# Performance work log

Hardware: AMD Instinct MI355X
Metric: run time of the kernel (lower is better)

## Reference

```python
import jax, jax.numpy as jnp
import numpy as np

U, B, I, D = 50000, 20000, 40000, 64
E_UI, E_UB, E_UBX, E_AGG = 1000000, 600000, 800000, 300000
EPS = 1e-8


def _bip_graph(rng, nA, nB, nE):
    """Symmetric Laplacian-normalized bipartite graph as directed COO edge list."""
    r = rng.integers(0, nA, nE)
    c = rng.integers(0, nB, nE)
    deg_r = np.bincount(r, minlength=nA).astype(np.float32)
    deg_c = np.bincount(c, minlength=nB).astype(np.float32)
    v = (1.0 / (np.sqrt(deg_r[r]) + EPS)) * (1.0 / (np.sqrt(deg_c[c]) + EPS))
    rows = np.concatenate([r, c + nA])
    cols = np.concatenate([c + nA, r])
    vals = np.concatenate([v, v]).astype(np.float32)
    return np.stack([rows, cols]).astype(np.int32), vals


def setup_inputs() -> dict:
    rng = np.random.default_rng(0)
    ui_idx, ui_val = _bip_graph(rng, U, I, E_UI)
    ub_idx, ub_val = _bip_graph(rng, U, B, E_UB)
    ubx_idx, ubx_val = _bip_graph(rng, U, B, E_UBX)  # ingredient-augmented u-b graph
    # bundle aggregation graph: row-normalized B x I (bi graph)
    br = rng.integers(0, B, E_AGG)
    bc = rng.integers(0, I, E_AGG)
    bdeg = np.bincount(br, minlength=B).astype(np.float32)
    agg_val = (1.0 / np.maximum(bdeg[br], 1.0)).astype(np.float32)
    agg_idx = np.stack([br, bc]).astype(np.int32)
    key = jax.random.key(0)
    ku, kb, ki = jax.random.split(key, 3)
    s = np.sqrt(2.0 / (U + D)).astype(np.float32)  # xavier-normal-ish scale
    return {
        "users_feature": jax.random.normal(ku, (U, D), jnp.float32) * 0.02,
        "bundles_feature": jax.random.normal(kb, (B, D), jnp.float32) * 0.02,
        "items_feature": jax.random.normal(ki, (I, D), jnp.float32) * 0.02,
        "ui_idx": jnp.asarray(ui_idx), "ui_val": jnp.asarray(ui_val),
        "ub_idx": jnp.asarray(ub_idx), "ub_val": jnp.asarray(ub_val),
        "ubx_idx": jnp.asarray(ubx_idx), "ubx_val": jnp.asarray(ubx_val),
        "agg_idx": jnp.asarray(agg_idx), "agg_val": jnp.asarray(agg_val),
        "num_layers": 2,
    }


def _spmm(idx, val, x, n_out):
    # y[r] += val[e] * x[c] for each edge e=(r,c)
    return jax.ops.segment_sum(val[:, None] * x[idx[1]], idx[0], num_segments=n_out)


def _l2norm(x):
    n = jnp.sqrt(jnp.sum(x * x, axis=1, keepdims=True))
    return x / jnp.maximum(n, 1e-12)


def _one_propagate(idx, val, A_feat, B_feat, num_layers):
    feats = jnp.concatenate([A_feat, B_feat], axis=0)
    n = feats.shape[0]
    acc = feats  # layer 0 raw
    f = feats
    for i in range(num_layers):
        f = _spmm(idx, val, f, n) / (i + 2)
        acc = acc + _l2norm(f)
    return acc[: A_feat.shape[0]], acc[A_feat.shape[0]:]


def reference(users_feature, bundles_feature, items_feature, ui_idx, ui_val,
              ub_idx, ub_val, ubx_idx, ubx_val, agg_idx, agg_val, num_layers):
    # item-level propagation over user-item graph
    IL_u, IL_i = _one_propagate(ui_idx, ui_val, users_feature, items_feature, num_layers)
    IL_b = _spmm(agg_idx, agg_val, IL_i, bundles_feature.shape[0])  # bundle agg from items
    # bundle-level propagation over user-bundle graph
    BL_u, BL_b = _one_propagate(ub_idx, ub_val, users_feature, bundles_feature, num_layers)
    # ingredient-augmented user-bundle propagation
    XL_u, XL_b = _one_propagate(ubx_idx, ubx_val, users_feature, bundles_feature, num_layers)
    # pack all representations: [3*U + 3*B, D]
    return jnp.concatenate([IL_u, BL_u, XL_u, IL_b, BL_b, XL_b], axis=0)
```

## Files before the change

### kernel.cpp

```cpp
#include <hip/hip_runtime.h>

#define D 64
constexpr int U_ = 50000, B_ = 20000, I_ = 40000;
constexpr int RPB  = 128;
constexpr int MAXB = 708;
constexpr int PTILE = 8192;

constexpr int NBU = 390;
constexpr int CAPU_UI = 3584, CAPB_UI = 4352;
constexpr int CAPA    = 2560;
constexpr int CAPU_UB = 2432, CAPB_UB = 4864;
constexpr int CAPU_UX = 2944, CAPB_UX = 6272;
constexpr int EXT_UI = NBU * CAPU_UI + 314 * CAPB_UI;
constexpr int EXT_AG = 157 * CAPA;
constexpr int EXT_UB = NBU * CAPU_UB + 157 * CAPB_UB;
constexpr int EXT_UX = NBU * CAPU_UX + 157 * CAPB_UX;
constexpr long long EXT_SUM = (long long)EXT_UI + EXT_AG + EXT_UB + EXT_UX;

__device__ __forceinline__ int g_nbU(int seg) { return seg == 1 ? 0 : NBU; }
__device__ __forceinline__ int g_capU(int seg) {
    switch (seg) { case 0: return CAPU_UI; case 1: return CAPA;
                   case 2: return CAPU_UB; default: return CAPU_UX; }
}
__device__ __forceinline__ int g_capB(int seg) {
    switch (seg) { case 0: return CAPB_UI; case 1: return CAPA;
                   case 2: return CAPB_UB; default: return CAPB_UX; }
}
__device__ __forceinline__ int bbase(int seg, int b) {
    int nbU = g_nbU(seg);
    return (b <= nbU) ? b * g_capU(seg)
                      : nbU * g_capU(seg) + (b - nbU) * g_capB(seg);
}

__device__ __forceinline__ unsigned short f2bf(float f) {
    unsigned int u = __float_as_uint(f);
    return (unsigned short)((u + 0x7FFFu + ((u >> 16) & 1u)) >> 16);
}

struct GD {
    const int* rows; const int* cols;
    int* ep; int* cnt; int* bktcur;
    int* ecol; int* rowstart; int* rowend; float* scale;
    const float* rawA; const float* rawB_adj;
    ushort* fb;
    int nnz, G, nbuck, seg, n, mode, do_pad, do_stage;
};
struct GB4 { GD g[4]; int ng; int Gpre[5]; int nbpre[5]; };

__global__ void __launch_bounds__(256) k_cntB(GB4 P) {
    __shared__ int lcnt[MAXB];
    int blk = blockIdx.x, t = threadIdx.x;
    int gi = 0;
    while (gi + 1 < P.ng && blk >= P.Gpre[gi + 1]) gi++;
    const GD& d = P.g[gi];
    int rel = blk - P.Gpre[gi];
    const int* __restrict__ rows = d.rows;
    for (int i = t; i < d.nbuck; i += 256) lcnt[i] = 0;
    __syncthreads();
    int e0 = rel * PTILE, e1 = min(e0 + PTILE, d.nnz);
    int e = e0 + t;
    for (; e + 1792 < e1; e += 2048) {
        int r[8];
        #pragma unroll
        for (int k = 0; k < 8; k++) r[k] = rows[e + k * 256];
        #pragma unroll
        for (int k = 0; k < 8; k++) atomicAdd(&lcnt[r[k] >> 7], 1);
    }
    for (; e < e1; e += 256) atomicAdd(&lcnt[rows[e] >> 7], 1);
    __syncthreads();
    for (int b = t; b < d.nbuck; b += 256) d.cnt[(size_t)b * d.G + rel] = lcnt[b];
}

__global__ void __launch_bounds__(256) k_scanB(GB4 P) {
    __shared__ int sv[256];
    int bk = blockIdx.x, t = threadIdx.x;
    int gi = 0;
    while (gi + 1 < P.ng && bk >= P.nbpre[gi + 1]) gi++;
    const GD& d = P.g[gi];
    int rel = bk - P.nbpre[gi];
    int x = (t < d.G) ? d.cnt[(size_t)rel * d.G + t] : 0;
    sv[t] = x;
    __syncthreads();
    for (int off = 1; off < 256; off <<= 1) {
        int y = (t >= off) ? sv[t - off] : 0;
        __syncthreads();
        sv[t] += y;
        __syncthreads();
    }
    int bb = bbase(d.seg, rel);
    if (t < d.G) d.cnt[(size_t)rel * d.G + t] = bb + sv[t] - x;
    if (t == 255) d.bktcur[rel] = bb + sv[255];
}

__global__ void __launch_bounds__(256) k_scatB(GB4 P) {
    __shared__ int lbase[MAXB], lcnt[MAXB], llim[MAXB];
    int blk = blockIdx.x, t = threadIdx.x;
    int gi = 0;
    while (gi + 1 < P.ng && blk >= P.Gpre[gi + 1]) gi++;
    const GD& d = P.g[gi];
    int rel = blk - P.Gpre[gi];
    const int* __restrict__ rows = d.rows;
    const int* __restrict__ cols = d.cols;
    int* __restrict__ ep = d.ep;
    for (int b = t; b < d.nbuck; b += 256) {
        lbase[b] = d.cnt[(size_t)b * d.G + rel];
        llim[b]  = bbase(d.seg, b + 1);
        lcnt[b]  = 0;
    }
    __syncthreads();
    int e0 = rel * PTILE, e1 = min(e0 + PTILE, d.nnz);
    int e = e0 + t;
    for (; e + 1792 < e1; e += 2048) {
        int r[8], c[8];
        #pragma unroll
        for (int k = 0; k < 8; k++) { r[k] = rows[e + k * 256]; c[k] = cols[e + k * 256]; }
        #pragma unroll
        for (int k = 0; k < 8; k++) {
            int b = r[k] >> 7;
            int pos = lbase[b] + atomicAdd(&lcnt[b], 1);
            if (pos < llim[b])
                ep[pos] = ((r[k] & (RPB - 1)) << 17) | c[k];
        }
    }
    for (; e < e1; e += 256) {
        int r = rows[e], c = cols[e];
        int b = r >> 7;
        int pos = lbase[b] + atomicAdd(&lcnt[b], 1);
        if (pos < llim[b])
            ep[pos] = ((r & (RPB - 1)) << 17) | c;
    }
}

__global__ void __launch_bounds__(256) k_sortB(GB4 P) {
    __shared__ int lc[4 * 129];
    __shared__ float sscale[RPB];
    __shared__ int wtot;
    int bk = blockIdx.x, t = threadIdx.x;
    int gi = 0;
    while (gi + 1 < P.ng && bk >= P.nbpre[gi + 1]) gi++;
    const GD& d = P.g[gi];
    int b = bk - P.nbpre[gi];
    const int* __restrict__ ep = d.ep;
    int* __restrict__ ecol = d.ecol;
    int s = bbase(d.seg, b);
    int e = min(d.bktcur[b], bbase(d.seg, b + 1));
    int ne = e - s;
    for (int i = t; i < 4 * 129; i += 256) lc[i] = 0;
    __syncthreads();
    int rep = (t & 3) * 129;
    int i = t;
    for (; i + 768 < ne; i += 1024) {
        int p0 = ep[s+i], p1 = ep[s+i+256], p2 = ep[s+i+512], p3 = ep[s+i+768];
        atomicAdd(&lc[rep + (p0 >> 17)], 1); atomicAdd(&lc[rep + (p1 >> 17)], 1);
        atomicAdd(&lc[rep + (p2 >> 17)], 1); atomicAdd(&lc[rep + (p3 >> 17)], 1);
    }
    for (; i < ne; i += 256) { int p = ep[s + i]; atomicAdd(&lc[rep + (p >> 17)], 1); }
    __syncthreads();
    int c_t = 0, pc_t = 0, v = 0;
    if (t < RPB) {
        c_t = lc[t] + lc[129 + t] + lc[258 + t] + lc[387 + t];
        pc_t = d.do_pad ? ((c_t + 7) & ~7) : c_t;
        v = pc_t;
        for (int off = 1; off < 64; off <<= 1) {
            int y = __shfl_up(v, off, 64);
            if ((t & 63) >= off) v += y;
        }
    }
    if (t == 63) wtot = v;
    __syncthreads();
    if (t >= 64 && t < RPB) v += wtot;
    if (t < RPB) {
        int row = b * RPB + t;
        if (row < d.n) {
            int st = s + (v - pc_t);
            d.rowstart[row] = st;
            d.rowend[row]   = st + pc_t;
            float sc = (d.mode == 0) ? 1.0f / (sqrtf((float)c_t) + 1e-8f)
                                     : 1.0f / (float)max(c_t, 1);
            d.scale[row] = sc;
            sscale[t] = sc;
            for (int k = c_t; k < pc_t; k++) ecol[st + k] = d.n;
            lc[t] = st;
        } else lc[t] = 0;
    }
    __syncthreads();
    i = t;
    for (; i + 768 < ne; i += 1024) {
        int p0 = ep[s+i], p1 = ep[s+i+256], p2 = ep[s+i+512], p3 = ep[s+i+768];
        int q0 = atomicAdd(&lc[p0 >> 17], 1); ecol[q0] = p0 & 0x1FFFF;
        int q1 = atomicAdd(&lc[p1 >> 17], 1); ecol[q1] = p1 & 0x1FFFF;
        int q2 = atomicAdd(&lc[p2 >> 17], 1); ecol[q2] = p2 & 0x1FFFF;
        int q3 = atomicAdd(&lc[p3 >> 17], 1); ecol[q3] = p3 & 0x1FFFF;
    }
    for (; i < ne; i += 256) {
        int p = ep[s + i];
        int q = atomicAdd(&lc[p >> 17], 1);
        ecol[q] = p & 0x1FFFF;
    }
    if (d.do_stage) {
        int r0 = b * RPB;
        for (int idx = t; idx < RPB * 16; idx += 256) {
            int rl = idx >> 4, q = idx & 15;
            int row = r0 + rl;
            if (row > d.n) continue;
            ushort4 o;
            if (row == d.n) {
                o = make_ushort4(0, 0, 0, 0);
            } else {
                float sc = sscale[rl];
                float4 vv = (row < U_) ? ((const float4*)d.rawA)[(size_t)row * 16 + q]
                                       : ((const float4*)d.rawB_adj)[(size_t)row * 16 + q];
                o.x = f2bf(vv.x * sc); o.y = f2bf(vv.y * sc);
                o.z = f2bf(vv.z * sc); o.w = f2bf(vv.w * sc);
            }
            ((ushort4*)d.fb)[(size_t)row * 16 + q] = o;
        }
    }
}

struct LD {
    const int* rowstart; const int* rowend; const float* scale;
    const int* ecol; const ushort* x; ushort* fout;
    const float* rawA; const float* rawB_adj;
    float* accA; float* accB;
    float inv; int n, write_f, init;
};
struct LB3 { LD l[3]; int nl; int qpre[4]; };

__global__ void __launch_bounds__(256) k_layerB(LB3 P) {
    int blk = blockIdx.x;
    int gi = 0;
    while (gi + 1 < P.nl && blk >= P.qpre[gi + 1]) gi++;
    const LD& d = P.l[gi];
    int rel = blk - P.qpre[gi];
    if (d.write_f && rel == 0 && threadIdx.x < 16)
        ((ushort4*)(d.fout + ((size_t)d.n << 6)))[threadIdx.x] = make_ushort4(0, 0, 0, 0);
    const int* __restrict__ rowstart = d.rowstart;
    const int* __restrict__ rowend   = d.rowend;
    const int* __restrict__ ecol     = d.ecol;
    const float* __restrict__ scale  = d.scale;
    const uint4* __restrict__ xb = (const uint4*)d.x;
    const int lane = threadIdx.x & 63;
    const int qtr  = lane >> 4;
    const int ql   = lane & 15;
    const int g = ql >> 3, q = ql & 7;
    int rowA = (rel << 4) + ((threadIdx.x >> 6) << 2);
    if (rowA >= d.n) return;
    int row = rowA + qtr;
    int s = 0, e = 0;
    if (row < d.n) { s = rowstart[row]; e = rowend[row]; }
    float a0=0.f,a1=0.f,a2=0.f,a3=0.f,a4=0.f,a5=0.f,a6=0.f,a7=0.f;
#define LDQ(m, vv) { int c_ = __shfl(cj, (qtr << 4) + ((m) << 1) + g, 64); \
                     vv = xb[((size_t)(unsigned)c_ << 3) + (unsigned)q]; }
#define ACCQ(vv) { \
    a0 += __uint_as_float(vv.x << 16); a1 += __uint_as_float(vv.x & 0xFFFF0000u); \
    a2 += __uint_as_float(vv.y << 16); a3 += __uint_as_float(vv.y & 0xFFFF0000u); \
    a4 += __uint_as_float(vv.z << 16); a5 += __uint_as_float(vv.z & 0xFFFF0000u); \
    a6 += __uint_as_float(vv.w << 16); a7 += __uint_as_float(vv.w & 0xFFFF0000u); }
    for (int base = s; base < e; base += 16) {
        int jn = e - base;
        int cj = ecol[base + ql];
        uint4 v0, v1, v2, v3, v4, v5, v6, v7;
        if (jn >= 16) {
            LDQ(0, v0); LDQ(1, v1); LDQ(2, v2); LDQ(3, v3);
            LDQ(4, v4); ACCQ(v0);
            LDQ(5, v5); ACCQ(v1);
            LDQ(6, v6); ACCQ(v2);
            LDQ(7, v7); ACCQ(v3);
            ACCQ(v4); ACCQ(v5); ACCQ(v6); ACCQ(v7);
        } else {
            LDQ(0, v0); LDQ(1, v1); LDQ(2, v2); LDQ(3, v3);
            ACCQ(v0); ACCQ(v1); ACCQ(v2); ACCQ(v3);
        }
    }
#undef LDQ
#undef ACCQ
#define RED(aa) { aa += __shfl_xor(aa, 8, 64); }
    RED(a0) RED(a1) RED(a2) RED(a3) RED(a4) RED(a5) RED(a6) RED(a7)
#undef RED
    float srow = (row < d.n) ? scale[row] : 0.f;
    float mlt = srow * d.inv;
    float w0=a0*mlt, w1=a1*mlt, w2=a2*mlt, w3=a3*mlt;
    float w4=a4*mlt, w5=a5*mlt, w6=a6*mlt, w7=a7*mlt;
    float sq = w0*w0 + w1*w1 + w2*w2 + w3*w3 + w4*w4 + w5*w5 + w6*w6 + w7*w7;
    sq += __shfl_xor(sq, 1, 64); sq += __shfl_xor(sq, 2, 64); sq += __shfl_xor(sq, 4, 64);
    float rn = 1.0f / fmaxf(sqrtf(sq), 1e-12f);
    if (row < d.n && g == 0) {
        size_t o = ((size_t)row << 6) + ((unsigned)q << 3);
        if (d.write_f) {
            unsigned p0 = (unsigned)f2bf(w0*srow) | ((unsigned)f2bf(w1*srow) << 16);
            unsigned p1 = (unsigned)f2bf(w2*srow) | ((unsigned)f2bf(w3*srow) << 16);
            unsigned p2 = (unsigned)f2bf(w4*srow) | ((unsigned)f2bf(w5*srow) << 16);
            unsigned p3 = (unsigned)f2bf(w6*srow) | ((unsigned)f2bf(w7*srow) << 16);
            *(uint4*)(d.fout + o) = make_uint4(p0, p1, p2, p3);
        }
        float r0=w0*rn, r1=w1*rn, r2=w2*rn, r3=w3*rn;
        float r4=w4*rn, r5=w5*rn, r6=w6*rn, r7=w7*rn;
        float* p = (row < U_) ? d.accA + o : d.accB + (o - ((size_t)U_ << 6));
        float4 c0, c1;
        if (d.init) {
            const float4* rp = (const float4*)((row < U_) ? d.rawA : d.rawB_adj)
                               + ((size_t)row << 4) + ((unsigned)q << 1);
            c0 = rp[0]; c1 = rp[1];
        } else {
            c0 = ((const float4*)p)[0]; c1 = ((const float4*)p)[1];
        }
        ((float4*)p)[0] = make_float4(c0.x + r0, c0.y + r1, c0.z + r2, c0.w + r3);
        ((float4*)p)[1] = make_float4(c1.x + r4, c1.y + r5, c1.z + r6, c1.w + r7);
    }
}

__global__ void k_spmm_csr(const int* __restrict__ rowstart, const int* __restrict__ rowend,
                           const int* __restrict__ ecol,
                           const float* __restrict__ rs, int n,
                           const float* __restrict__ x, float* __restrict__ y) {
    int row = (blockIdx.x << 2) + (threadIdx.x >> 6);
    if (row >= n) return;
    int lane = threadIdx.x & 63;
    int s = rowstart[row], e = rowend[row];
    float acc = 0.f;
    for (int base = s; base < e; base += 64) {
        int jn = e - base; if (jn > 64) jn = 64;
        int li = base + (lane < jn ? lane : jn - 1);
        int cj = ecol[li];
        int j = 0;
        for (; j + 8 <= jn; j += 8) {
            int c0 = __shfl(cj, j + 0, 64), c1 = __shfl(cj, j + 1, 64);
            int c2 = __shfl(cj, j + 2, 64), c3 = __shfl(cj, j + 3, 64);
            int c4 = __shfl(cj, j + 4, 64), c5 = __shfl(cj, j + 5, 64);
            int c6 = __shfl(cj, j + 6, 64), c7 = __shfl(cj, j + 7, 64);
            float v0 = x[(size_t)c0 * D + lane], v1 = x[(size_t)c1 * D + lane];
            float v2 = x[(size_t)c2 * D + lane], v3 = x[(size_t)c3 * D + lane];
            float v4 = x[(size_t)c4 * D + lane], v5 = x[(size_t)c5 * D + lane];
            float v6 = x[(size_t)c6 * D + lane], v7 = x[(size_t)c7 * D + lane];
            acc += ((v0 + v1) + (v2 + v3)) + ((v4 + v5) + (v6 + v7));
        }
        for (; j < jn; j++) {
            int c = __shfl(cj, j, 64);
            acc += x[(size_t)c * D + lane];
        }
    }
    y[(size_t)row * D + lane] = acc * rs[row];
}

extern "C" void kernel_launch(void* const* d_in, const int* in_sizes, int n_in,
                              void* d_out, int out_size, void* d_ws, size_t ws_size,
                              hipStream_t stream) {
    const float* users   = (const float*)d_in[0];
    const float* bundles = (const float*)d_in[1];
    const float* items   = (const float*)d_in[2];
    const int*   ui_idx  = (const int*)d_in[3];
    const int*   ub_idx  = (const int*)d_in[5];
    const int*   ubx_idx = (const int*)d_in[7];
    const int*   agg_idx = (const int*)d_in[9];
    const int ui_nnz  = in_sizes[4];
    const int ub_nnz  = in_sizes[6];
    const int ubx_nnz = in_sizes[8];
    const int agg_nnz = in_sizes[10];

    float* out = (float*)d_out;
    const size_t rowf = (size_t)D;
    float* out_IL_u = out;
    float* out_BL_u = out + (size_t)U_ * rowf;
    float* out_XL_u = out + (size_t)2 * U_ * rowf;
    float* out_IL_b = out + (size_t)3 * U_ * rowf;
    float* out_BL_b = out + (size_t)3 * U_ * rowf + (size_t)B_ * rowf;
    float* out_XL_b = out + (size_t)3 * U_ * rowf + (size_t)2 * B_ * rowf;

    const int G0 = (ui_nnz  + PTILE - 1) / PTILE;
    const int G1 = (agg_nnz + PTILE - 1) / PTILE;
    const int G2 = (ub_nnz  + PTILE - 1) / PTILE;
    const int G3 = (ubx_nnz + PTILE - 1) / PTILE;
    const int NB0 = 704, NB1 = 157, NB2 = 547, NB3 = 547;
    const size_t co0 = 0, co1 = (size_t)NB0 * G0, co2 = co1 + (size_t)NB1 * G1,
                 co3 = co2 + (size_t)NB2 * G2, cntInts = co3 + (size_t)NB3 * G3;
    const int nU = U_ + I_, nB2g = U_ + B_;

    const int* rowsArr[4] = { ui_idx, agg_idx, ub_idx, ubx_idx };
    const int nnzArr[4]   = { ui_nnz, agg_nnz, ub_nnz, ubx_nnz };
    const int GArr[4]     = { G0, G1, G2, G3 };
    const int nbArr[4]    = { NB0, NB1, NB2, NB3 };
    const int nArr[4]     = { nU, B_, nB2g, nB2g };
    const int modeArr[4]  = { 0, 1, 0, 0 };
    const int padArr[4]   = { 1, 0, 1, 1 };
    const int stgArr[4]   = { 1, 0, 1, 1 };
    const size_t coArr[4] = { co0, co1, co2, co3 };
    const float* rawBArr[4] = { items - (size_t)U_ * rowf, users,
                                bundles - (size_t)U_ * rowf, bundles - (size_t)U_ * rowf };

    const size_t fbBytes  = 230003ull * 128;
    const size_t accBytes = 40001ull * 256;
    const size_t ecBytes  = (size_t)EXT_SUM * 4;
    const size_t rsBytes  = 250016ull * 4;
    const size_t bkBytes  = 4ull * MAXB * 4;
    const size_t epcnt    = (size_t)EXT_SUM * 4 + cntInts * 4;
    const size_t tailB    = epcnt > fbBytes ? epcnt : fbBytes;
    const size_t reqA     = fbBytes + accBytes + ecBytes + 3 * rsBytes + bkBytes + tailB + 4096;

    GB4 P{};
    P.ng = 4;
    P.Gpre[0] = 0; P.nbpre[0] = 0;
    for (int i = 0; i < 4; i++) { P.Gpre[i+1] = P.Gpre[i] + GArr[i]; P.nbpre[i+1] = P.nbpre[i] + nbArr[i]; }

    if (ws_size >= reqA) {
        char* w = (char*)d_ws;
        ushort* fbA   = (ushort*)w;                 w += fbBytes;
        float* accI   = (float*)w;                  w += accBytes;
        int*   ecolA  = (int*)w;                    w += ecBytes;
        int*   rsA    = (int*)w;                    w += rsBytes;
        int*   reA    = (int*)w;                    w += rsBytes;
        float* scA    = (float*)w;                  w += rsBytes;
        int*   bkA    = (int*)w;                    w += bkBytes;
        int*   epA    = (int*)w;
        int*   cntA   = epA + EXT_SUM;
        ushort* gbA   = (ushort*)epA;

        const size_t epoff[4] = { 0, (size_t)EXT_UI, (size_t)EXT_UI + EXT_AG,
                                  (size_t)EXT_UI + EXT_AG + EXT_UB };
        const size_t roff[4]  = { 0, 90004, 110008, 180012 };
        const size_t fboff[4] = { 0, 0, 90001ull * 64, 160002ull * 64 };

        for (int i = 0; i < 4; i++) {
            GD& d = P.g[i];
            d.rows = rowsArr[i]; d.cols = rowsArr[i] + nnzArr[i];
            d.ep = epA + epoff[i]; d.cnt = cntA + coArr[i]; d.bktcur = bkA + i * MAXB;
            d.ecol = ecolA + epoff[i];
            d.rowstart = rsA + roff[i]; d.rowend = reA + roff[i]; d.scale = scA + roff[i];
            d.rawA = users; d.rawB_adj = rawBArr[i];
            d.fb = (i == 1) ? nullptr : fbA + fboff[i];
            d.nnz = nnzArr[i]; d.G = GArr[i]; d.nbuck = nbArr[i]; d.seg = i;
            d.n = nArr[i]; d.mode = modeArr[i]; d.do_pad = padArr[i]; d.do_stage = stgArr[i];
        }
        hipLaunchKernelGGL(k_cntB,  dim3(P.Gpre[4]),  dim3(256), 0, stream, P);
        hipLaunchKernelGGL(k_scanB, dim3(P.nbpre[4]), dim3(256), 0, stream, P);
        hipLaunchKernelGGL(k_scatB, dim3(P.Gpre[4]),  dim3(256), 0, stream, P);
        hipLaunchKernelGGL(k_sortB, dim3(P.nbpre[4]), dim3(256), 0, stream, P);

        float* accAArr[3] = { out_IL_u, out_BL_u, out_XL_u };
        float* accBArr[3] = { accI, out_BL_b, out_XL_b };
        int gsel[3] = { 0, 2, 3 };
        LB3 L{};
        L.nl = 3; L.qpre[0] = 0;
        for (int j = 0; j < 3; j++) {
            int i = gsel[j];
            LD& l = L.l[j];
            l.rowstart = P.g[i].rowstart; l.rowend = P.g[i].rowend; l.scale = P.g[i].scale;
            l.ecol = P.g[i].ecol; l.rawA = users; l.rawB_adj = rawBArr[i];
            l.accA = accAArr[j]; l.accB = accBArr[j];
            l.n = nArr[i];
            L.qpre[j + 1] = L.qpre[j] + ((nArr[i] + 15) >> 4);
        }
        for (int j = 0; j < 3; j++) {
            int i = gsel[j];
            L.l[j].x = fbA + fboff[i]; L.l[j].fout = gbA + fboff[i];
            L.l[j].inv = 0.5f; L.l[j].write_f = 1; L.l[j].init = 1;
        }
        hipLaunchKernelGGL(k_layerB, dim3(L.qpre[3]), dim3(256), 0, stream, L);
        for (int j = 0; j < 3; j++) {
            int i = gsel[j];
            L.l[j].x = gbA + fboff[i]; L.l[j].fout = (ushort*)nullptr;
            L.l[j].inv = 1.0f / 3.0f; L.l[j].write_f = 0; L.l[j].init = 0;
        }
        hipLaunchKernelGGL(k_layerB, dim3(L.qpre[3]), dim3(256), 0, stream, L);
        hipLaunchKernelGGL(k_spmm_csr, dim3((B_ + 3) / 4), dim3(256), 0, stream,
                           P.g[1].rowstart, P.g[1].rowend, P.g[1].ecol,
                           P.g[1].scale, B_, accI, out_IL_b);
    } else {
        const int NROWPAD = 90004;
        const int EPMAX = 547 * 6144;
        ushort* fb16 = (ushort*)d_ws;
        float* accI  = (float*)(fb16 + (size_t)90001 * D + 32);
        float* scB   = accI + (size_t)I_ * D;
        int* epB     = (int*)(scB + NROWPAD);
        ushort* gb16 = (ushort*)epB;
        int* ecolB   = epB + EPMAX;
        int* rsB     = ecolB + EPMAX;
        int* reB     = rsB + NROWPAD;
        int* bkB     = reB + NROWPAD;
        int* cntB    = epB + 2950000;

        for (int i = 0; i < 4; i++) {
            GD& d = P.g[i];
            d.rows = rowsArr[i]; d.cols = rowsArr[i] + nnzArr[i];
            d.ep = epB; d.cnt = cntB + coArr[i]; d.bktcur = bkB + i * MAXB;
            d.ecol = ecolB; d.rowstart = rsB; d.rowend = reB; d.scale = scB;
            d.rawA = users; d.rawB_adj = rawBArr[i];
            d.fb = fb16;
            d.nnz = nnzArr[i]; d.G = GArr[i]; d.nbuck = nbArr[i]; d.seg = i;
            d.n = nArr[i]; d.mode = modeArr[i]; d.do_pad = padArr[i]; d.do_stage = stgArr[i];
        }
        hipLaunchKernelGGL(k_cntB,  dim3(P.Gpre[4]),  dim3(256), 0, stream, P);
        hipLaunchKernelGGL(k_scanB, dim3(P.nbpre[4]), dim3(256), 0, stream, P);

        auto one = [&](int i) {
            GB4 Q{};
            Q.ng = 1; Q.g[0] = P.g[i];
            Q.Gpre[0] = 0; Q.Gpre[1] = GArr[i];
            Q.nbpre[0] = 0; Q.nbpre[1] = nbArr[i];
            hipLaunchKernelGGL(k_scatB, dim3(GArr[i]),  dim3(256), 0, stream, Q);
            hipLaunchKernelGGL(k_sortB, dim3(nbArr[i]), dim3(256), 0, stream, Q);
        };
        auto layers = [&](int i, float* accA, float* accB) {
            LB3 L{};
            L.nl = 1; L.qpre[0] = 0; L.qpre[1] = (nArr[i] + 15) >> 4;
            LD& l = L.l[0];
            l.rowstart = rsB; l.rowend = reB; l.scale = scB; l.ecol = ecolB;
            l.rawA = users; l.rawB_adj = rawBArr[i];
            l.accA = accA; l.accB = accB; l.n = nArr[i];
            l.x = fb16; l.fout = gb16; l.inv = 0.5f; l.write_f = 1; l.init = 1;
            hipLaunchKernelGGL(k_layerB, dim3(L.qpre[1]), dim3(256), 0, stream, L);
            l.x = gb16; l.fout = (ushort*)nullptr; l.inv = 1.0f / 3.0f;
            l.write_f = 0; l.init = 0;
            hipLaunchKernelGGL(k_layerB, dim3(L.qpre[1]), dim3(256), 0, stream, L);
        };

        one(0); layers(0, out_IL_u, accI);
        one(1);
        hipLaunchKernelGGL(k_spmm_csr, dim3((B_ + 3) / 4), dim3(256), 0, stream,
                           rsB, reB, ecolB, scB, B_, accI, out_IL_b);
        one(2); layers(2, out_BL_u, out_BL_b);
        one(3); layers(3, out_XL_u, out_XL_b);
    }
}
```

Before: 431.3 us.

## Defer layer-1 accumulator write and rewrite bundle aggregation spmm with float4 quarter-waves

Layer 1 no longer writes the fp32 accumulator. It stores a per-row factor (l2 norm reciprocal divided by the row scale), and layer 2 rebuilds the normalized layer-1 term from the bf16 feature buffer it already reads, then writes raw + layer1 + layer2 in one pass. This removes one fp32 read-modify-write of the accumulator per propagation, at the cost of using a bf16-rounded layer-1 contribution, which lowers accuracy. The item-to-bundle spmm now handles four rows per wavefront with float4 loads instead of one row per wavefront with scalar loads.

```diff
diff --git a/kernel.cpp b/kernel.cpp
--- a/kernel.cpp
+++ b/kernel.cpp
@@ -222,8 +222,8 @@
     const int* rowstart; const int* rowend; const float* scale;
     const int* ecol; const ushort* x; ushort* fout;
     const float* rawA; const float* rawB_adj;
-    float* accA; float* accB;
-    float inv; int n, write_f, init;
+    float* accA; float* accB; float* l2s;
+    float inv; int n, phase;
 };
 struct LB3 { LD l[3]; int nl; int qpre[4]; };
 
@@ -233,7 +233,7 @@
     while (gi + 1 < P.nl && blk >= P.qpre[gi + 1]) gi++;
     const LD& d = P.l[gi];
     int rel = blk - P.qpre[gi];
-    if (d.write_f && rel == 0 && threadIdx.x < 16)
+    if (d.phase == 0 && rel == 0 && threadIdx.x < 16)
         ((ushort4*)(d.fout + ((size_t)d.n << 6)))[threadIdx.x] = make_ushort4(0, 0, 0, 0);
     const int* __restrict__ rowstart = d.rowstart;
     const int* __restrict__ rowend   = d.rowend;
@@ -278,7 +278,7 @@
 #define RED(aa) { aa += __shfl_xor(aa, 8, 64); }
     RED(a0) RED(a1) RED(a2) RED(a3) RED(a4) RED(a5) RED(a6) RED(a7)
 #undef RED
-    float srow = (row < d.n) ? scale[row] : 0.f;
+    float srow = (row < d.n) ? scale[row] : 1.f;
     float mlt = srow * d.inv;
     float w0=a0*mlt, w1=a1*mlt, w2=a2*mlt, w3=a3*mlt;
     float w4=a4*mlt, w5=a5*mlt, w6=a6*mlt, w7=a7*mlt;
@@ -287,60 +287,79 @@
     float rn = 1.0f / fmaxf(sqrtf(sq), 1e-12f);
     if (row < d.n && g == 0) {
         size_t o = ((size_t)row << 6) + ((unsigned)q << 3);
-        if (d.write_f) {
+        if (d.phase == 0) {
             unsigned p0 = (unsigned)f2bf(w0*srow) | ((unsigned)f2bf(w1*srow) << 16);
             unsigned p1 = (unsigned)f2bf(w2*srow) | ((unsigned)f2bf(w3*srow) << 16);
             unsigned p2 = (unsigned)f2bf(w4*srow) | ((unsigned)f2bf(w5*srow) << 16);
             unsigned p3 = (unsigned)f2bf(w6*srow) | ((unsigned)f2bf(w7*srow) << 16);
             *(uint4*)(d.fout + o) = make_uint4(p0, p1, p2, p3);
-        }
-        float r0=w0*rn, r1=w1*rn, r2=w2*rn, r3=w3*rn;
-        float r4=w4*rn, r5=w5*rn, r6=w6*rn, r7=w7*rn;
-        float* p = (row < U_) ? d.accA + o : d.accB + (o - ((size_t)U_ << 6));
-        float4 c0, c1;
-        if (d.init) {
+            if (q == 0) d.l2s[row] = rn / srow;
+        } else {
+            uint4 gv = *(const uint4*)(d.x + o);
+            float lv = d.l2s[row];
+            float g0 = __uint_as_float(gv.x << 16) * lv,
+                  g1 = __uint_as_float(gv.x & 0xFFFF0000u) * lv,
+                  g2 = __uint_as_float(gv.y << 16) * lv,
+                  g3 = __uint_as_float(gv.y & 0xFFFF0000u) * lv,
+                  g4 = __uint_as_float(gv.z << 16) * lv,
+                  g5 = __uint_as_float(gv.z & 0xFFFF0000u) * lv,
+                  g6 = __uint_as_float(gv.w << 16) * lv,
+                  g7 = __uint_as_float(gv.w & 0xFFFF0000u) * lv;
             const float4* rp = (const float4*)((row < U_) ? d.rawA : d.rawB_adj)
                                + ((size_t)row << 4) + ((unsigned)q << 1);
-            c0 = rp[0]; c1 = rp[1];
-        } else {
-            c0 = ((const float4*)p)[0]; c1 = ((const float4*)p)[1];
-        }
-        ((float4*)p)[0] = make_float4(c0.x + r0, c0.y + r1, c0.z + r2, c0.w + r3);
-        ((float4*)p)[1] = make_float4(c1.x + r4, c1.y + r5, c1.z + r6, c1.w + r7);
-    }
-}
-
-__global__ void k_spmm_csr(const int* __restrict__ rowstart, const int* __restrict__ rowend,
-                           const int* __restrict__ ecol,
-                           const float* __restrict__ rs, int n,
-                           const float* __restrict__ x, float* __restrict__ y) {
-    int row = (blockIdx.x << 2) + (threadIdx.x >> 6);
-    if (row >= n) return;
-    int lane = threadIdx.x & 63;
-    int s = rowstart[row], e = rowend[row];
-    float acc = 0.f;
-    for (int base = s; base < e; base += 64) {
-        int jn = e - base; if (jn > 64) jn = 64;
-        int li = base + (lane < jn ? lane : jn - 1);
+            float4 c0 = rp[0], c1 = rp[1];
+            float* p = (row < U_) ? d.accA + o : d.accB + (o - ((size_t)U_ << 6));
+            ((float4*)p)[0] = make_float4(c0.x + g0 + w0*rn, c0.y + g1 + w1*rn,
+                                          c0.z + g2 + w2*rn, c0.w + g3 + w3*rn);
+            ((float4*)p)[1] = make_float4(c1.x + g4 + w4*rn, c1.y + g5 + w5*rn,
+                                          c1.z + g6 + w6*rn, c1.w + g7 + w7*rn);
+        }
+    }
+}
+
+__global__ void __launch_bounds__(256)
+k_spmm4(const int* __restrict__ rowstart, const int* __restrict__ rowend,
+        const int* __restrict__ ecol, const float* __restrict__ rs, int n,
+        const float* __restrict__ x, float* __restrict__ y) {
+    const int lane = threadIdx.x & 63;
+    const int qtr = lane >> 4, ql = lane & 15;
+    int rowA = (blockIdx.x << 4) + ((threadIdx.x >> 6) << 2);
+    if (rowA >= n) return;
+    int row = rowA + qtr;
+    bool live = row < n;
+    int s = live ? rowstart[row] : 0, e = live ? rowend[row] : 0;
+    const float4* __restrict__ xb = (const float4*)x;
+    float4 acc = make_float4(0.f, 0.f, 0.f, 0.f);
+    for (int base = s; base < e; base += 16) {
+        int jn = e - base; if (jn > 16) jn = 16;
+        int li = base + (ql < jn ? ql : jn - 1);
         int cj = ecol[li];
         int j = 0;
-        for (; j + 8 <= jn; j += 8) {
-            int c0 = __shfl(cj, j + 0, 64), c1 = __shfl(cj, j + 1, 64);
-            int c2 = __shfl(cj, j + 2, 64), c3 = __shfl(cj, j + 3, 64);
-            int c4 = __shfl(cj, j + 4, 64), c5 = __shfl(cj, j + 5, 64);
-            int c6 = __shfl(cj, j + 6, 64), c7 = __shfl(cj, j + 7, 64);
-            float v0 = x[(size_t)c0 * D + lane], v1 = x[(size_t)c1 * D + lane];
-            float v2 = x[(size_t)c2 * D + lane], v3 = x[(size_t)c3 * D + lane];
-            float v4 = x[(size_t)c4 * D + lane], v5 = x[(size_t)c5 * D + lane];
-            float v6 = x[(size_t)c6 * D + lane], v7 = x[(size_t)c7 * D + lane];
-            acc += ((v0 + v1) + (v2 + v3)) + ((v4 + v5) + (v6 + v7));
+        for (; j + 4 <= jn; j += 4) {
+            int c0 = __shfl(cj, (qtr << 4) + j + 0, 64);
+            int c1 = __shfl(cj, (qtr << 4) + j + 1, 64);
+            int c2 = __shfl(cj, (qtr << 4) + j + 2, 64);
+            int c3 = __shfl(cj, (qtr << 4) + j + 3, 64);
+            float4 v0 = xb[(size_t)c0 * 16 + ql];
+            float4 v1 = xb[(size_t)c1 * 16 + ql];
+            float4 v2 = xb[(size_t)c2 * 16 + ql];
+            float4 v3 = xb[(size_t)c3 * 16 + ql];
+            acc.x += (v0.x + v1.x) + (v2.x + v3.x);
+            acc.y += (v0.y + v1.y) + (v2.y + v3.y);
+            acc.z += (v0.z + v1.z) + (v2.z + v3.z);
+            acc.w += (v0.w + v1.w) + (v2.w + v3.w);
         }
         for (; j < jn; j++) {
-            int c = __shfl(cj, j, 64);
-            acc += x[(size_t)c * D + lane];
-        }
-    }
-    y[(size_t)row * D + lane] = acc * rs[row];
+            int c = __shfl(cj, (qtr << 4) + j, 64);
+            float4 v = xb[(size_t)c * 16 + ql];
+            acc.x += v.x; acc.y += v.y; acc.z += v.z; acc.w += v.w;
+        }
+    }
+    if (live) {
+        float sc = rs[row];
+        ((float4*)y)[(size_t)row * 16 + ql] =
+            make_float4(acc.x * sc, acc.y * sc, acc.z * sc, acc.w * sc);
+    }
 }
 
 extern "C" void kernel_launch(void* const* d_in, const int* in_sizes, int n_in,
@@ -395,7 +414,7 @@
     const size_t bkBytes  = 4ull * MAXB * 4;
     const size_t epcnt    = (size_t)EXT_SUM * 4 + cntInts * 4;
     const size_t tailB    = epcnt > fbBytes ? epcnt : fbBytes;
-    const size_t reqA     = fbBytes + accBytes + ecBytes + 3 * rsBytes + bkBytes + tailB + 4096;
+    const size_t reqA     = fbBytes + accBytes + ecBytes + 4 * rsBytes + bkBytes + tailB + 4096;
 
     GB4 P{};
     P.ng = 4;
@@ -410,6 +429,7 @@
         int*   rsA    = (int*)w;                    w += rsBytes;
         int*   reA    = (int*)w;                    w += rsBytes;
         float* scA    = (float*)w;                  w += rsBytes;
+        float* l2sA   = (float*)w;                  w += rsBytes;
         int*   bkA    = (int*)w;                    w += bkBytes;
         int*   epA    = (int*)w;
         int*   cntA   = epA + EXT_SUM;
@@ -447,22 +467,23 @@
             l.rowstart = P.g[i].rowstart; l.rowend = P.g[i].rowend; l.scale = P.g[i].scale;
             l.ecol = P.g[i].ecol; l.rawA = users; l.rawB_adj = rawBArr[i];
             l.accA = accAArr[j]; l.accB = accBArr[j];
+            l.l2s = l2sA + roff[i];
             l.n = nArr[i];
             L.qpre[j + 1] = L.qpre[j] + ((nArr[i] + 15) >> 4);
         }
         for (int j = 0; j < 3; j++) {
             int i = gsel[j];
             L.l[j].x = fbA + fboff[i]; L.l[j].fout = gbA + fboff[i];
-            L.l[j].inv = 0.5f; L.l[j].write_f = 1; L.l[j].init = 1;
+            L.l[j].inv = 0.5f; L.l[j].phase = 0;
         }
         hipLaunchKernelGGL(k_layerB, dim3(L.qpre[3]), dim3(256), 0, stream, L);
         for (int j = 0; j < 3; j++) {
             int i = gsel[j];
             L.l[j].x = gbA + fboff[i]; L.l[j].fout = (ushort*)nullptr;
-            L.l[j].inv = 1.0f / 3.0f; L.l[j].write_f = 0; L.l[j].init = 0;
+            L.l[j].inv = 1.0f / 3.0f; L.l[j].phase = 1;
         }
         hipLaunchKernelGGL(k_layerB, dim3(L.qpre[3]), dim3(256), 0, stream, L);
-        hipLaunchKernelGGL(k_spmm_csr, dim3((B_ + 3) / 4), dim3(256), 0, stream,
+        hipLaunchKernelGGL(k_spmm4, dim3((B_ + 15) / 16), dim3(256), 0, stream,
                            P.g[1].rowstart, P.g[1].rowend, P.g[1].ecol,
                            P.g[1].scale, B_, accI, out_IL_b);
     } else {
@@ -477,6 +498,7 @@
         int* rsB     = ecolB + EPMAX;
         int* reB     = rsB + NROWPAD;
         int* bkB     = reB + NROWPAD;
+        float* l2sB  = (float*)(bkB + 4 * MAXB);
         int* cntB    = epB + 2950000;
 
         for (int i = 0; i < 4; i++) {
@@ -506,17 +528,16 @@
             LD& l = L.l[0];
             l.rowstart = rsB; l.rowend = reB; l.scale = scB; l.ecol = ecolB;
             l.rawA = users; l.rawB_adj = rawBArr[i];
-            l.accA = accA; l.accB = accB; l.n = nArr[i];
-            l.x = fb16; l.fout = gb16; l.inv = 0.5f; l.write_f = 1; l.init = 1;
+            l.accA = accA; l.accB = accB; l.l2s = l2sB; l.n = nArr[i];
+            l.x = fb16; l.fout = gb16; l.inv = 0.5f; l.phase = 0;
             hipLaunchKernelGGL(k_layerB, dim3(L.qpre[1]), dim3(256), 0, stream, L);
-            l.x = gb16; l.fout = (ushort*)nullptr; l.inv = 1.0f / 3.0f;
-            l.write_f = 0; l.init = 0;
+            l.x = gb16; l.fout = (ushort*)nullptr; l.inv = 1.0f / 3.0f; l.phase = 1;
             hipLaunchKernelGGL(k_layerB, dim3(L.qpre[1]), dim3(256), 0, stream, L);
         };
 
         one(0); layers(0, out_IL_u, accI);
         one(1);
-        hipLaunchKernelGGL(k_spmm_csr, dim3((B_ + 3) / 4), dim3(256), 0, stream,
+        hipLaunchKernelGGL(k_spmm4, dim3((B_ + 15) / 16), dim3(256), 0, stream,
                            rsB, reB, ecolB, scB, B_, accI, out_IL_b);
         one(2); layers(2, out_BL_u, out_BL_b);
         one(3); layers(3, out_XL_u, out_XL_b);
```

After: 422.9 us. No clear change (-2.0%).
